# Kernel tuning notes

Hardware: AMD Instinct MI355X
Metric: run time of the kernel (lower is better)

## Reference

```python
import jax, jax.numpy as jnp
import numpy as np

N_NODES = 50000
N_EDGES = 800000
IN_F, HID, OUT_F = 256, 128, 8
N_LAYERS = 3
N_GRAPHS = 256
NEG_SLOPE = 0.2  # PyG GATConv default negative_slope


def setup_inputs() -> dict:
    key = jax.random.key(0)
    ks = jax.random.split(key, 16)
    inp = {
        "x": jax.random.normal(ks[0], (N_NODES, IN_F), dtype=jnp.float32),
        "edge_index": jax.random.randint(ks[1], (2, N_EDGES), 0, N_NODES, dtype=jnp.int64),
        "edge_attr": jax.random.normal(ks[2], (N_EDGES, 8), dtype=jnp.float32),
        "batch": jnp.sort(jax.random.randint(ks[3], (N_NODES,), 0, N_GRAPHS, dtype=jnp.int64)),
    }
    # Per-layer GATConv params (heads=1): lin weight, att_src, att_dst, bias.
    dims = [(IN_F, HID), (HID, HID), (HID, HID)]
    for l, (di, do) in enumerate(dims):
        s = 1.0 / np.sqrt(di)
        inp[f"W{l}"] = jax.random.uniform(ks[4 + l], (di, do), jnp.float32, -s, s)
        inp[f"a_src{l}"] = jax.random.normal(ks[7 + l], (do,), jnp.float32) * 0.1
        inp[f"a_dst{l}"] = jax.random.normal(ks[10 + l], (do,), jnp.float32) * 0.1
        inp[f"b{l}"] = jnp.zeros((do,), jnp.float32)
    s = 1.0 / np.sqrt(HID)
    inp["lin_w"] = jax.random.uniform(ks[13], (HID, OUT_F), jnp.float32, -s, s)
    inp["lin_b"] = jnp.zeros((OUT_F,), jnp.float32)
    return inp


def _segment_softmax(logits, seg, num_segments):
    m = jax.ops.segment_max(logits, seg, num_segments=num_segments)
    e = jnp.exp(logits - m[seg])
    s = jax.ops.segment_sum(e, seg, num_segments=num_segments)
    return e / s[seg]


def _gat_layer(x, src, dst, W, a_src, a_dst, b):
    h = x @ W                              # [N, H]
    alpha_s = h @ a_src                    # [N]
    alpha_d = h @ a_dst                    # [N]
    logits = jax.nn.leaky_relu(alpha_s[src] + alpha_d[dst], NEG_SLOPE)  # [E]
    alpha = _segment_softmax(logits, dst, N_NODES)                      # [E]
    out = jax.ops.segment_sum(alpha[:, None] * h[src], dst, num_segments=N_NODES)
    return out + b


def reference(x, edge_index, edge_attr, batch,
              W0, a_src0, a_dst0, b0,
              W1, a_src1, a_dst1, b1,
              W2, a_src2, a_dst2, b2,
              lin_w, lin_b):
    src, dst = edge_index[0], edge_index[1]
    # is_edge_attr=False: edge_attr unused, matching the else-branch.
    h = _gat_layer(x, src, dst, W0, a_src0, a_dst0, b0)
    h = jax.nn.relu(h)
    h = _gat_layer(h, src, dst, W1, a_src1, a_dst1, b1)
    h = jax.nn.relu(h)
    h = _gat_layer(h, src, dst, W2, a_src2, a_dst2, b2)  # last layer: no relu
    # global_mean_pool
    sums = jax.ops.segment_sum(h, batch, num_segments=N_GRAPHS)
    cnt = jax.ops.segment_sum(jnp.ones((N_NODES,), h.dtype), batch, num_segments=N_GRAPHS)
    pooled = sums / jnp.maximum(cnt, 1.0)[:, None]
    # Dropout is identity in eval mode.
    return pooled @ lin_w + lin_b  # logits [G, OUT_F]
```

## Files before the change

### kernel.cpp

```cpp
#include <hip/hip_runtime.h>
#include <cstdint>
#include <cstddef>

#define N_NODES_C  50000
#define N_EDGES_C  800000
#define IN_F_C     256
#define HID_C      128
#define N_GRAPHS_C 256
#define NEG_SLOPE_C 0.2f
#define SCAN_NB    ((N_NODES_C + 255) / 256)
#define POOL_SPLIT 8
#define SCAT_BUCKETS 8
#define SCAT_CHUNKS  256

typedef _Float16 f16x8 __attribute__((ext_vector_type(8)));
typedef float    f32x4 __attribute__((ext_vector_type(4)));

__global__ void hist_rank_kernel(const int* __restrict__ dst, int* __restrict__ deg,
                                 int* __restrict__ rank, int E) {
    int e = blockIdx.x * blockDim.x + threadIdx.x;
    if (e < E) rank[e] = atomicAdd(&deg[dst[e]], 1);
}

__global__ __launch_bounds__(256) void scan1_kernel(const int* __restrict__ deg,
                                                    int* __restrict__ bsum, int n) {
    int i = blockIdx.x * 256 + threadIdx.x;
    int lane = threadIdx.x & 63;
    int w = threadIdx.x >> 6;
    int v = (i < n) ? deg[i] : 0;
    #pragma unroll
    for (int off = 32; off >= 1; off >>= 1) v += __shfl_xor(v, off);
    __shared__ int ws_[4];
    if (lane == 0) ws_[w] = v;
    __syncthreads();
    if (threadIdx.x == 0) bsum[blockIdx.x] = ws_[0] + ws_[1] + ws_[2] + ws_[3];
}

__global__ __launch_bounds__(256) void scan2_kernel(int* __restrict__ bsum, int nb) {
    int t = threadIdx.x;
    int lane = t & 63;
    int w = t >> 6;
    int orig = (t < nb) ? bsum[t] : 0;
    int v = orig;
    #pragma unroll
    for (int off = 1; off < 64; off <<= 1) {
        int u = __shfl_up(v, off);
        if (lane >= off) v += u;
    }
    __shared__ int wsum[4];
    if (lane == 63) wsum[w] = v;
    __syncthreads();
    int add = 0;
    for (int i = 0; i < w; ++i) add += wsum[i];
    if (t < nb) bsum[t] = v + add - orig;
}

__global__ __launch_bounds__(256) void scan3_kernel(const int* __restrict__ deg,
                                                    const int* __restrict__ boff,
                                                    int* __restrict__ row_start, int n) {
    int i = blockIdx.x * 256 + threadIdx.x;
    int lane = threadIdx.x & 63;
    int w = threadIdx.x >> 6;
    int d = (i < n) ? deg[i] : 0;
    int v = d;
    #pragma unroll
    for (int off = 1; off < 64; off <<= 1) {
        int u = __shfl_up(v, off);
        if (lane >= off) v += u;
    }
    __shared__ int wsum[4];
    if (lane == 63) wsum[w] = v;
    __syncthreads();
    int add = boff[blockIdx.x];
    for (int k = 0; k < w; ++k) add += wsum[k];
    int excl = v - d + add;
    if (i < n) {
        row_start[i] = excl;
        if (i == n - 1) row_start[n] = excl + d;
    }
}

__global__ __launch_bounds__(256) void scatter_bucket_kernel(
    const int* __restrict__ src, const int* __restrict__ dst,
    const int* __restrict__ rank, const int* __restrict__ row_start,
    int* __restrict__ csr_src, int E)
{
    const int bucket = blockIdx.x & (SCAT_BUCKETS - 1);
    const int chunk  = blockIdx.x / SCAT_BUCKETS;
    constexpr int NPB = (N_NODES_C + SCAT_BUCKETS - 1) / SCAT_BUCKETS;
    const int lo = bucket * NPB;
    const int hi = min(lo + NPB, N_NODES_C);
    const int per = (E + SCAT_CHUNKS - 1) / SCAT_CHUNKS;
    const int e0 = chunk * per;
    const int e1 = min(e0 + per, E);
    for (int e = e0 + (int)threadIdx.x; e < e1; e += 256) {
        int d = dst[e];
        if (d >= lo && d < hi) {
            csr_src[row_start[d] + rank[e]] = src[e];
        }
    }
}

__global__ void convert_w_kernel(const float* __restrict__ W,
                                 _Float16* __restrict__ wt_hi,
                                 _Float16* __restrict__ wt_lo, int K) {
    int id = blockIdx.x * 256 + threadIdx.x;
    if (id >= K * 128) return;
    int c = id & 127;
    int k = id >> 7;
    float w = W[(size_t)k * 128 + c];
    _Float16 h = (_Float16)w;
    _Float16 l = (_Float16)(w - (float)h);
    wt_hi[(size_t)c * K + k] = h;
    wt_lo[(size_t)c * K + k] = l;
}

template <int K, bool RELU>
__global__ __launch_bounds__(256) void gemm_mfma_kernel(
    const float* __restrict__ X,
    const _Float16* __restrict__ WTh, const _Float16* __restrict__ WTl,
    const float* __restrict__ a_src, const float* __restrict__ a_dst,
    _Float16* __restrict__ Hh, float* __restrict__ alpha_s, float* __restrict__ alpha_d,
    int n_rows)
{
    constexpr int NS = K / 32;
    __shared__ _Float16 XsH[2][64 * 32];
    __shared__ _Float16 XsL[2][64 * 32];
    __shared__ float aps[4][64];
    __shared__ float apd[4][64];

    const int t = threadIdx.x;
    const int row0 = blockIdx.x * 64;
    const int lane = t & 63;
    const int wv = t >> 6;
    const int l15 = lane & 15;
    const int l4 = lane >> 4;
    const int wcol = wv * 32;

    const int sr = t >> 2;
    const int skg = t & 3;
    const int sgrow = row0 + sr;
    const int sslot = skg ^ (sr & 3);
    const int sldsoff = sr * 32 + sslot * 8;
    const bool srow_ok = (sgrow < n_rows);
    const float* __restrict__ srowp = X + (size_t)sgrow * K + skg * 8;

    f32x4 acc[4][2];
    #pragma unroll
    for (int mt = 0; mt < 4; ++mt)
        #pragma unroll
        for (int nt = 0; nt < 2; ++nt)
            acc[mt][nt] = (f32x4){0.f, 0.f, 0.f, 0.f};

    {
        float4 xa = make_float4(0.f, 0.f, 0.f, 0.f), xb = xa;
        if (srow_ok) {
            xa = *reinterpret_cast<const float4*>(srowp);
            xb = *reinterpret_cast<const float4*>(srowp + 4);
        }
        float v[8] = {xa.x, xa.y, xa.z, xa.w, xb.x, xb.y, xb.z, xb.w};
        f16x8 hi, lo;
        #pragma unroll
        for (int i = 0; i < 8; ++i) {
            float x = v[i];
            if (RELU) x = fmaxf(x, 0.f);
            _Float16 h = (_Float16)x;
            hi[i] = h;
            lo[i] = (_Float16)(x - (float)h);
        }
        *reinterpret_cast<f16x8*>(&XsH[0][sldsoff]) = hi;
        *reinterpret_cast<f16x8*>(&XsL[0][sldsoff]) = lo;
    }
    __syncthreads();

    int cur = 0;
    for (int step = 0; step < NS; ++step) {
        const int k0 = step * 32;
        float4 nxa = make_float4(0.f, 0.f, 0.f, 0.f), nxb = nxa;
        const bool hasNext = (step + 1 < NS);
        if (hasNext && srow_ok) {
            nxa = *reinterpret_cast<const float4*>(srowp + k0 + 32);
            nxb = *reinterpret_cast<const float4*>(srowp + k0 + 36);
        }
        f16x8 bh[2], bl[2];
        #pragma unroll
        for (int nt = 0; nt < 2; ++nt) {
            const size_t bo = (size_t)(wcol + nt * 16 + l15) * K + k0 + l4 * 8;
            bh[nt] = *reinterpret_cast<const f16x8*>(WTh + bo);
            bl[nt] = *reinterpret_cast<const f16x8*>(WTl + bo);
        }
        const int aslot = l4 ^ (l15 & 3);
        f16x8 ah[4], al[4];
        #pragma unroll
        for (int mt = 0; mt < 4; ++mt) {
            const int off = (mt * 16 + l15) * 32 + aslot * 8;
            ah[mt] = *reinterpret_cast<const f16x8*>(&XsH[cur][off]);
            al[mt] = *reinterpret_cast<const f16x8*>(&XsL[cur][off]);
        }
        #pragma unroll
        for (int mt = 0; mt < 4; ++mt)
            #pragma unroll
            for (int nt = 0; nt < 2; ++nt) {
                acc[mt][nt] = __builtin_amdgcn_mfma_f32_16x16x32_f16(ah[mt], bh[nt], acc[mt][nt], 0, 0, 0);
                acc[mt][nt] = __builtin_amdgcn_mfma_f32_16x16x32_f16(ah[mt], bl[nt], acc[mt][nt], 0, 0, 0);
                acc[mt][nt] = __builtin_amdgcn_mfma_f32_16x16x32_f16(al[mt], bh[nt], acc[mt][nt], 0, 0, 0);
            }
        if (hasNext) {
            float v[8] = {nxa.x, nxa.y, nxa.z, nxa.w, nxb.x, nxb.y, nxb.z, nxb.w};
            f16x8 hi, lo;
            #pragma unroll
            for (int i = 0; i < 8; ++i) {
                float x = v[i];
                if (RELU) x = fmaxf(x, 0.f);
                _Float16 h = (_Float16)x;
                hi[i] = h;
                lo[i] = (_Float16)(x - (float)h);
            }
            *reinterpret_cast<f16x8*>(&XsH[cur ^ 1][sldsoff]) = hi;
            *reinterpret_cast<f16x8*>(&XsL[cur ^ 1][sldsoff]) = lo;
        }
        __syncthreads();
        cur ^= 1;
    }

    const float as0 = a_src[wcol + l15];
    const float as1 = a_src[wcol + 16 + l15];
    const float ad0 = a_dst[wcol + l15];
    const float ad1 = a_dst[wcol + 16 + l15];

    #pragma unroll
    for (int mt = 0; mt < 4; ++mt) {
        #pragma unroll
        for (int reg = 0; reg < 4; ++reg) {
            const int lrow = mt * 16 + l4 * 4 + reg;
            const int grow = row0 + lrow;
            if (grow < n_rows) {
                Hh[(size_t)grow * 128 + wcol + l15]      = (_Float16)acc[mt][0][reg];
                Hh[(size_t)grow * 128 + wcol + 16 + l15] = (_Float16)acc[mt][1][reg];
            }
            float s = acc[mt][0][reg] * as0 + acc[mt][1][reg] * as1;
            float d = acc[mt][0][reg] * ad0 + acc[mt][1][reg] * ad1;
            #pragma unroll
            for (int off = 8; off >= 1; off >>= 1) {
                s += __shfl_xor(s, off);
                d += __shfl_xor(d, off);
            }
            if (l15 == 0) {
                aps[wv][lrow] = s;
                apd[wv][lrow] = d;
            }
        }
    }
    __syncthreads();
    if (t < 64) {
        const int grow = row0 + t;
        if (grow < n_rows)
            alpha_s[grow] = aps[0][t] + aps[1][t] + aps[2][t] + aps[3][t];
    } else if (t < 128) {
        const int tt = t - 64;
        const int grow = row0 + tt;
        if (grow < n_rows)
            alpha_d[grow] = apd[0][tt] + apd[1][tt] + apd[2][tt] + apd[3][tt];
    }
}

__global__ __launch_bounds__(256) void aggregate_kernel(
    const _Float16* __restrict__ Hh, const float* __restrict__ alpha_s,
    const float* __restrict__ alpha_d, const int* __restrict__ row_start,
    const int* __restrict__ csr_src, const float* __restrict__ bias,
    float* __restrict__ OUT, int n_nodes)
{
    int wid = (blockIdx.x * blockDim.x + threadIdx.x) >> 6;
    int lane = threadIdx.x & 63;
    if (wid >= n_nodes) return;

    int e0 = row_start[wid], e1 = row_start[wid + 1];
    float ad = alpha_d[wid];

    const int grp = lane >> 4;
    const int l16 = lane & 15;
    const _Float16* __restrict__ Hc = Hh + l16 * 8;

    float S = 0.f;
    float accA[8], accB[8], accC[8], accD[8];
    #pragma unroll
    for (int q = 0; q < 8; ++q) { accA[q] = 0.f; accB[q] = 0.f; accC[q] = 0.f; accD[q] = 0.f; }

    for (int base = e0; base < e1; base += 64) {
        int e = base + lane;
        float w = 0.f;
        int s = 0;
        if (e < e1) {
            s = csr_src[e];
            float z = alpha_s[s] + ad;
            z = (z >= 0.f) ? z : NEG_SLOPE_C * z;
            w = __expf(z);
        }
        float ws = w;
        #pragma unroll
        for (int off = 32; off >= 1; off >>= 1) ws += __shfl_xor(ws, off);
        S += ws;
        int cnt = min(64, e1 - base);

        for (int jj = 0; jj < cnt; jj += 16) {
            int i0 = jj + grp;
            int i1 = jj + 4 + grp;
            int i2 = jj + 8 + grp;
            int i3 = jj + 12 + grp;
            float w0 = __shfl(w, i0 & 63);
            int   s0 = __shfl(s, i0 & 63);
            float w1 = __shfl(w, i1 & 63);
            int   s1 = __shfl(s, i1 & 63);
            float w2 = __shfl(w, i2 & 63);
            int   s2 = __shfl(s, i2 & 63);
            float w3 = __shfl(w, i3 & 63);
            int   s3 = __shfl(s, i3 & 63);
            w0 = (i0 < cnt) ? w0 : 0.f;
            w1 = (i1 < cnt) ? w1 : 0.f;
            w2 = (i2 < cnt) ? w2 : 0.f;
            w3 = (i3 < cnt) ? w3 : 0.f;
            f16x8 h0 = *reinterpret_cast<const f16x8*>(Hc + (size_t)s0 * 128);
            f16x8 h1 = *reinterpret_cast<const f16x8*>(Hc + (size_t)s1 * 128);
            f16x8 h2 = *reinterpret_cast<const f16x8*>(Hc + (size_t)s2 * 128);
            f16x8 h3 = *reinterpret_cast<const f16x8*>(Hc + (size_t)s3 * 128);
            #pragma unroll
            for (int q = 0; q < 8; ++q) accA[q] = fmaf(w0, (float)h0[q], accA[q]);
            #pragma unroll
            for (int q = 0; q < 8; ++q) accB[q] = fmaf(w1, (float)h1[q], accB[q]);
            #pragma unroll
            for (int q = 0; q < 8; ++q) accC[q] = fmaf(w2, (float)h2[q], accC[q]);
            #pragma unroll
            for (int q = 0; q < 8; ++q) accD[q] = fmaf(w3, (float)h3[q], accD[q]);
        }
    }

    float acc[8];
    #pragma unroll
    for (int q = 0; q < 8; ++q) acc[q] = (accA[q] + accB[q]) + (accC[q] + accD[q]);
    #pragma unroll
    for (int q = 0; q < 8; ++q) {
        acc[q] += __shfl_xor(acc[q], 16);
        acc[q] += __shfl_xor(acc[q], 32);
    }

    float inv = (e1 > e0) ? (1.f / S) : 0.f;
    if (grp == 0) {
        float4 b0 = *reinterpret_cast<const float4*>(bias + l16 * 8);
        float4 b1 = *reinterpret_cast<const float4*>(bias + l16 * 8 + 4);
        float4 o0, o1;
        o0.x = acc[0] * inv + b0.x;
        o0.y = acc[1] * inv + b0.y;
        o0.z = acc[2] * inv + b0.z;
        o0.w = acc[3] * inv + b0.w;
        o1.x = acc[4] * inv + b1.x;
        o1.y = acc[5] * inv + b1.y;
        o1.z = acc[6] * inv + b1.z;
        o1.w = acc[7] * inv + b1.w;
        *reinterpret_cast<float4*>(OUT + (size_t)wid * 128 + l16 * 8)     = o0;
        *reinterpret_cast<float4*>(OUT + (size_t)wid * 128 + l16 * 8 + 4) = o1;
    }
}

__global__ void graph_ranges_kernel(const int* __restrict__ batch, int n_nodes,
                                    int n_graphs, int* __restrict__ gstart) {
    int g = blockIdx.x * blockDim.x + threadIdx.x;
    if (g > n_graphs) return;
    int lo = 0, hi = n_nodes;
    while (lo < hi) {
        int mid = (lo + hi) >> 1;
        if (batch[mid] < g) lo = mid + 1; else hi = mid;
    }
    gstart[g] = lo;
}

__global__ __launch_bounds__(128) void pool_partial_kernel(
    const float* __restrict__ X, const int* __restrict__ gstart,
    float* __restrict__ partial)
{
    int g = blockIdx.x >> 3;
    int split = blockIdx.x & 7;
    int c = threadIdx.x;
    int s = gstart[g], e = gstart[g + 1];
    int len = e - s;
    int i0 = s + (len * split) / POOL_SPLIT;
    int i1 = s + (len * (split + 1)) / POOL_SPLIT;
    float acc = 0.f;
    for (int i = i0; i < i1; ++i) acc += X[(size_t)i * 128 + c];
    partial[(size_t)blockIdx.x * 128 + c] = acc;
}

__global__ __launch_bounds__(128) void pool_final_kernel(
    const float* __restrict__ partial, const int* __restrict__ gstart,
    const float* __restrict__ lin_w, const float* __restrict__ lin_b,
    float* __restrict__ out)
{
    int g = blockIdx.x;
    int c = threadIdx.x;
    float acc = 0.f;
    #pragma unroll
    for (int sp = 0; sp < POOL_SPLIT; ++sp)
        acc += partial[(size_t)(g * POOL_SPLIT + sp) * 128 + c];
    float cnt = (float)(gstart[g + 1] - gstart[g]);
    float pooled = acc / fmaxf(cnt, 1.0f);
    __shared__ float p[128];
    p[c] = pooled;
    __syncthreads();
    if (c < 8) {
        float o = lin_b[c];
        for (int k = 0; k < 128; ++k) o += p[k] * lin_w[k * 8 + c];
        out[g * 8 + c] = o;
    }
}

extern "C" void kernel_launch(void* const* d_in, const int* in_sizes, int n_in,
                              void* d_out, int out_size, void* d_ws, size_t ws_size,
                              hipStream_t stream)
{
    const float* x     = (const float*)d_in[0];
    const int*   ei    = (const int*)d_in[1];
    const int*   batch = (const int*)d_in[3];
    const float* W[3]   = {(const float*)d_in[4],  (const float*)d_in[8],  (const float*)d_in[12]};
    const float* asr[3] = {(const float*)d_in[5],  (const float*)d_in[9],  (const float*)d_in[13]};
    const float* adt[3] = {(const float*)d_in[6],  (const float*)d_in[10], (const float*)d_in[14]};
    const float* bia[3] = {(const float*)d_in[7],  (const float*)d_in[11], (const float*)d_in[15]};
    const float* lin_w = (const float*)d_in[16];
    const float* lin_b = (const float*)d_in[17];
    float* out = (float*)d_out;

    char* ws = (char*)d_ws;
    size_t off = 0;
    auto carve = [&](size_t bytes) {
        void* p = ws + off;
        off = (off + bytes + 255) & ~(size_t)255;
        return p;
    };
    _Float16* Hh    = (_Float16*)carve((size_t)N_NODES_C * 128 * 2);
    float* bufB     = (float*)carve((size_t)N_NODES_C * 128 * 4);
    float* alpha_s  = (float*)carve((size_t)N_NODES_C * 4);
    float* alpha_d  = (float*)carve((size_t)N_NODES_C * 4);
    int*   deg      = (int*)carve((size_t)N_NODES_C * 4);
    int*   row_start= (int*)carve((size_t)(N_NODES_C + 1) * 4);
    int*   rank     = (int*)carve((size_t)N_EDGES_C * 4);
    int*   csr_src  = (int*)carve((size_t)N_EDGES_C * 4);
    int*   gstart   = (int*)carve((size_t)(N_GRAPHS_C + 1) * 4);
    int*   bsum     = (int*)carve((size_t)SCAN_NB * 4);
    float* ppart    = (float*)carve((size_t)N_GRAPHS_C * POOL_SPLIT * 128 * 4);
    _Float16* wt_h[3];
    _Float16* wt_l[3];
    wt_h[0] = (_Float16*)carve((size_t)128 * 256 * 2);
    wt_l[0] = (_Float16*)carve((size_t)128 * 256 * 2);
    wt_h[1] = (_Float16*)carve((size_t)128 * 128 * 2);
    wt_l[1] = (_Float16*)carve((size_t)128 * 128 * 2);
    wt_h[2] = (_Float16*)carve((size_t)128 * 128 * 2);
    wt_l[2] = (_Float16*)carve((size_t)128 * 128 * 2);

    const int* src = ei;
    const int* dst = ei + N_EDGES_C;

    hipMemsetAsync(deg, 0, (size_t)N_NODES_C * 4, stream);
    hist_rank_kernel<<<(N_EDGES_C + 255) / 256, 256, 0, stream>>>(dst, deg, rank, N_EDGES_C);
    scan1_kernel<<<SCAN_NB, 256, 0, stream>>>(deg, bsum, N_NODES_C);
    scan2_kernel<<<1, 256, 0, stream>>>(bsum, SCAN_NB);
    scan3_kernel<<<SCAN_NB, 256, 0, stream>>>(deg, bsum, row_start, N_NODES_C);
    scatter_bucket_kernel<<<SCAT_BUCKETS * SCAT_CHUNKS, 256, 0, stream>>>(
        src, dst, rank, row_start, csr_src, N_EDGES_C);
    graph_ranges_kernel<<<2, 256, 0, stream>>>(batch, N_NODES_C, N_GRAPHS_C, gstart);
    convert_w_kernel<<<(256 * 128 + 255) / 256, 256, 0, stream>>>(W[0], wt_h[0], wt_l[0], 256);
    convert_w_kernel<<<(128 * 128 + 255) / 256, 256, 0, stream>>>(W[1], wt_h[1], wt_l[1], 128);
    convert_w_kernel<<<(128 * 128 + 255) / 256, 256, 0, stream>>>(W[2], wt_h[2], wt_l[2], 128);

    const int gemm_grid = (N_NODES_C + 63) / 64;
    const int agg_grid  = (N_NODES_C + 3) / 4;

    gemm_mfma_kernel<IN_F_C, false><<<gemm_grid, 256, 0, stream>>>(
        x, wt_h[0], wt_l[0], asr[0], adt[0], Hh, alpha_s, alpha_d, N_NODES_C);
    aggregate_kernel<<<agg_grid, 256, 0, stream>>>(
        Hh, alpha_s, alpha_d, row_start, csr_src, bia[0], bufB, N_NODES_C);

    gemm_mfma_kernel<HID_C, true><<<gemm_grid, 256, 0, stream>>>(
        bufB, wt_h[1], wt_l[1], asr[1], adt[1], Hh, alpha_s, alpha_d, N_NODES_C);
    aggregate_kernel<<<agg_grid, 256, 0, stream>>>(
        Hh, alpha_s, alpha_d, row_start, csr_src, bia[1], bufB, N_NODES_C);

    gemm_mfma_kernel<HID_C, true><<<gemm_grid, 256, 0, stream>>>(
        bufB, wt_h[2], wt_l[2], asr[2], adt[2], Hh, alpha_s, alpha_d, N_NODES_C);
    aggregate_kernel<<<agg_grid, 256, 0, stream>>>(
        Hh, alpha_s, alpha_d, row_start, csr_src, bia[2], bufB, N_NODES_C);

    pool_partial_kernel<<<N_GRAPHS_C * POOL_SPLIT, 128, 0, stream>>>(bufB, gstart, ppart);
    pool_final_kernel<<<N_GRAPHS_C, 128, 0, stream>>>(ppart, gstart, lin_w, lin_b, out);
}
```

Measured before the change: 407.5 us.

## Process four destination nodes per wavefront in GAT aggregation

The aggregation kernel now assigns four consecutive destination nodes to each wavefront instead of one, interleaving their edge batches so that 16 independent gathered feature loads are in flight per iteration. The goal is more memory-level parallelism and amortised per-wave setup for low-degree nodes (average degree 16). In exchange it uses more registers (4x8 accumulators plus 16 loaded vectors), which may lower occupancy, and nodes with unequal degrees cause idle lanes up to the maximum count in each batch.

```diff
diff --git a/kernel.cpp b/kernel.cpp
--- a/kernel.cpp
+++ b/kernel.cpp
@@ -270,94 +270,133 @@
     const int* __restrict__ csr_src, const float* __restrict__ bias,
     float* __restrict__ OUT, int n_nodes)
 {
-    int wid = (blockIdx.x * blockDim.x + threadIdx.x) >> 6;
+    int wvid = (blockIdx.x * blockDim.x + threadIdx.x) >> 6;
     int lane = threadIdx.x & 63;
-    if (wid >= n_nodes) return;
-
-    int e0 = row_start[wid], e1 = row_start[wid + 1];
-    float ad = alpha_d[wid];
+    int n0 = wvid * 4;
+    if (n0 >= n_nodes) return;
 
     const int grp = lane >> 4;
     const int l16 = lane & 15;
     const _Float16* __restrict__ Hc = Hh + l16 * 8;
 
-    float S = 0.f;
-    float accA[8], accB[8], accC[8], accD[8];
-    #pragma unroll
-    for (int q = 0; q < 8; ++q) { accA[q] = 0.f; accB[q] = 0.f; accC[q] = 0.f; accD[q] = 0.f; }
-
-    for (int base = e0; base < e1; base += 64) {
-        int e = base + lane;
-        float w = 0.f;
-        int s = 0;
-        if (e < e1) {
-            s = csr_src[e];
-            float z = alpha_s[s] + ad;
-            z = (z >= 0.f) ? z : NEG_SLOPE_C * z;
-            w = __expf(z);
-        }
-        float ws = w;
-        #pragma unroll
-        for (int off = 32; off >= 1; off >>= 1) ws += __shfl_xor(ws, off);
-        S += ws;
-        int cnt = min(64, e1 - base);
-
-        for (int jj = 0; jj < cnt; jj += 16) {
-            int i0 = jj + grp;
-            int i1 = jj + 4 + grp;
-            int i2 = jj + 8 + grp;
-            int i3 = jj + 12 + grp;
-            float w0 = __shfl(w, i0 & 63);
-            int   s0 = __shfl(s, i0 & 63);
-            float w1 = __shfl(w, i1 & 63);
-            int   s1 = __shfl(s, i1 & 63);
-            float w2 = __shfl(w, i2 & 63);
-            int   s2 = __shfl(s, i2 & 63);
-            float w3 = __shfl(w, i3 & 63);
-            int   s3 = __shfl(s, i3 & 63);
-            w0 = (i0 < cnt) ? w0 : 0.f;
-            w1 = (i1 < cnt) ? w1 : 0.f;
-            w2 = (i2 < cnt) ? w2 : 0.f;
-            w3 = (i3 < cnt) ? w3 : 0.f;
-            f16x8 h0 = *reinterpret_cast<const f16x8*>(Hc + (size_t)s0 * 128);
-            f16x8 h1 = *reinterpret_cast<const f16x8*>(Hc + (size_t)s1 * 128);
-            f16x8 h2 = *reinterpret_cast<const f16x8*>(Hc + (size_t)s2 * 128);
-            f16x8 h3 = *reinterpret_cast<const f16x8*>(Hc + (size_t)s3 * 128);
-            #pragma unroll
-            for (int q = 0; q < 8; ++q) accA[q] = fmaf(w0, (float)h0[q], accA[q]);
-            #pragma unroll
-            for (int q = 0; q < 8; ++q) accB[q] = fmaf(w1, (float)h1[q], accB[q]);
-            #pragma unroll
-            for (int q = 0; q < 8; ++q) accC[q] = fmaf(w2, (float)h2[q], accC[q]);
-            #pragma unroll
-            for (int q = 0; q < 8; ++q) accD[q] = fmaf(w3, (float)h3[q], accD[q]);
-        }
-    }
-
-    float acc[8];
-    #pragma unroll
-    for (int q = 0; q < 8; ++q) acc[q] = (accA[q] + accB[q]) + (accC[q] + accD[q]);
-    #pragma unroll
-    for (int q = 0; q < 8; ++q) {
-        acc[q] += __shfl_xor(acc[q], 16);
-        acc[q] += __shfl_xor(acc[q], 32);
-    }
-
-    float inv = (e1 > e0) ? (1.f / S) : 0.f;
+    int rs[5];
+    #pragma unroll
+    for (int k = 0; k < 5; ++k) {
+        int idx = n0 + k;
+        rs[k] = row_start[idx < n_nodes ? idx : n_nodes];
+    }
+    float ad[4];
+    #pragma unroll
+    for (int k = 0; k < 4; ++k)
+        ad[k] = (n0 + k < n_nodes) ? alpha_d[n0 + k] : 0.f;
+
+    float S[4];
+    float acc[4][8];
+    #pragma unroll
+    for (int k = 0; k < 4; ++k) {
+        S[k] = 0.f;
+        #pragma unroll
+        for (int q = 0; q < 8; ++q) acc[k][q] = 0.f;
+    }
+
+    int base[4];
+    #pragma unroll
+    for (int k = 0; k < 4; ++k) base[k] = rs[k];
+
+    bool more = true;
+    while (more) {
+        int cnt[4];
+        float w[4];
+        int s[4];
+        #pragma unroll
+        for (int k = 0; k < 4; ++k) {
+            int rem = rs[k + 1] - base[k];
+            cnt[k] = rem > 0 ? (rem < 64 ? rem : 64) : 0;
+            float wk = 0.f;
+            int sk = 0;
+            if (lane < cnt[k]) {
+                sk = csr_src[base[k] + lane];
+                float z = alpha_s[sk] + ad[k];
+                z = (z >= 0.f) ? z : NEG_SLOPE_C * z;
+                wk = __expf(z);
+            }
+            w[k] = wk;
+            s[k] = sk;
+        }
+        #pragma unroll
+        for (int k = 0; k < 4; ++k) {
+            float r = w[k];
+            #pragma unroll
+            for (int off = 32; off >= 1; off >>= 1) r += __shfl_xor(r, off);
+            S[k] += r;
+        }
+
+        int cmax = max(max(cnt[0], cnt[1]), max(cnt[2], cnt[3]));
+        for (int jj = 0; jj < cmax; jj += 16) {
+            float bw[4][4];
+            int bs[4][4];
+            #pragma unroll
+            for (int k = 0; k < 4; ++k) {
+                #pragma unroll
+                for (int t = 0; t < 4; ++t) {
+                    int idx = jj + t * 4 + grp;
+                    float ww = __shfl(w[k], idx & 63);
+                    int ss = __shfl(s[k], idx & 63);
+                    bw[k][t] = (idx < cnt[k]) ? ww : 0.f;
+                    bs[k][t] = ss;
+                }
+            }
+            f16x8 h[4][4];
+            #pragma unroll
+            for (int k = 0; k < 4; ++k)
+                #pragma unroll
+                for (int t = 0; t < 4; ++t)
+                    h[k][t] = *reinterpret_cast<const f16x8*>(Hc + (size_t)bs[k][t] * 128);
+            #pragma unroll
+            for (int k = 0; k < 4; ++k)
+                #pragma unroll
+                for (int t = 0; t < 4; ++t)
+                    #pragma unroll
+                    for (int q = 0; q < 8; ++q)
+                        acc[k][q] = fmaf(bw[k][t], (float)h[k][t][q], acc[k][q]);
+        }
+        #pragma unroll
+        for (int k = 0; k < 4; ++k) base[k] += 64;
+        more = false;
+        #pragma unroll
+        for (int k = 0; k < 4; ++k) more = more || (base[k] < rs[k + 1]);
+    }
+
+    #pragma unroll
+    for (int k = 0; k < 4; ++k) {
+        #pragma unroll
+        for (int q = 0; q < 8; ++q) {
+            acc[k][q] += __shfl_xor(acc[k][q], 16);
+            acc[k][q] += __shfl_xor(acc[k][q], 32);
+        }
+    }
+
     if (grp == 0) {
         float4 b0 = *reinterpret_cast<const float4*>(bias + l16 * 8);
         float4 b1 = *reinterpret_cast<const float4*>(bias + l16 * 8 + 4);
-        float4 o0, o1;
-        o0.x = acc[0] * inv + b0.x;
-        o0.y = acc[1] * inv + b0.y;
-        o0.z = acc[2] * inv + b0.z;
-        o0.w = acc[3] * inv + b0.w;
-        o1.x = acc[4] * inv + b1.x;
-        o1.y = acc[5] * inv + b1.y;
-        o1.z = acc[6] * inv + b1.z;
-        o1.w = acc[7] * inv + b1.w;
-        *reinterpret_cast<float4*>(OUT + (size_t)wid * 128 + l16 * 8)     = o0;
-        *reinterpret_cast<float4*>(OUT + (size_t)wid * 128 + l16 * 8 + 4) = o1;
+        #pragma unroll
+        for (int k = 0; k < 4; ++k) {
+            int node = n0 + k;
+            if (node < n_nodes) {
+                float inv = (rs[k + 1] > rs[k]) ? (1.f / S[k]) : 0.f;
+                float4 o0, o1;
+                o0.x = acc[k][0] * inv + b0.x;
+                o0.y = acc[k][1] * inv + b0.y;
+                o0.z = acc[k][2] * inv + b0.z;
+                o0.w = acc[k][3] * inv + b0.w;
+                o1.x = acc[k][4] * inv + b1.x;
+                o1.y = acc[k][5] * inv + b1.y;
+                o1.z = acc[k][6] * inv + b1.z;
+                o1.w = acc[k][7] * inv + b1.w;
+                *reinterpret_cast<float4*>(OUT + (size_t)node * 128 + l16 * 8)     = o0;
+                *reinterpret_cast<float4*>(OUT + (size_t)node * 128 + l16 * 8 + 4) = o1;
+            }
+        }
     }
 }
 
@@ -470,7 +509,7 @@
     convert_w_kernel<<<(128 * 128 + 255) / 256, 256, 0, stream>>>(W[2], wt_h[2], wt_l[2], 128);
 
     const int gemm_grid = (N_NODES_C + 63) / 64;
-    const int agg_grid  = (N_NODES_C + 3) / 4;
+    const int agg_grid  = (N_NODES_C + 15) / 16;
 
     gemm_mfma_kernel<IN_F_C, false><<<gemm_grid, 256, 0, stream>>>(
         x, wt_h[0], wt_l[0], asr[0], adt[0], Hh, alpha_s, alpha_d, N_NODES_C);
```

Measured after the change: 433.6 us. 1.06x slower.
